# Kernel optimization log

Hardware: AMD Instinct MI355X
Metric: run time of the kernel (lower is better)

The kernel has to match this reference:

```python
import jax, jax.numpy as jnp
import numpy as np

LMAX = 6
NMAX = 5
RC = 6.0
N_ATOMS = 65536
L = LMAX + 1


def _solid_harmonics(p):
    """Orthonormal regular solid harmonics S_lm = r^l * Y_lm for one point p=(x,y,z),
    packed into an (L,L) matrix the way AutoForce's Ylm does:
      Y[l, l-m] = Re(S_lm)  (lower triangle incl. diagonal),
      Y[m-1, l] = Im(S_lm)  (strict upper triangle, m >= 1).
    These are polynomials in (x,y,z) so jacfwd gives exact analytic gradients."""
    x, y, z = p[0], p[1], p[2]
    r2 = x * x + y * y + z * z
    zero = jnp.zeros_like(x)
    re = {(0, 0): 0.28209479177387814 + zero}  # 1/sqrt(4*pi)
    im = {(0, 0): zero}
    for l in range(1, LMAX + 1):
        a = -float(np.sqrt((2 * l + 1) / (2.0 * l)))
        re[(l, l)] = a * (x * re[(l - 1, l - 1)] - y * im[(l - 1, l - 1)])
        im[(l, l)] = a * (x * im[(l - 1, l - 1)] + y * re[(l - 1, l - 1)])
        for m in range(l):
            A = float(np.sqrt((l * l - m * m) / ((2 * l - 1.0) * (2 * l + 1.0))))
            if l - 2 >= m:
                Ap = float(np.sqrt(((l - 1) ** 2 - m * m) / ((2 * l - 3.0) * (2 * l - 1.0))))
                re[(l, m)] = (z * re[(l - 1, m)] - Ap * r2 * re[(l - 2, m)]) / A
                im[(l, m)] = (z * im[(l - 1, m)] - Ap * r2 * im[(l - 2, m)]) / A
            else:
                re[(l, m)] = z * re[(l - 1, m)] / A
                im[(l, m)] = z * im[(l - 1, m)] / A
    rows = []
    for i in range(L):
        row = [re[(i, i - j)] if j <= i else im[(j, i + 1)] for j in range(L)]
        rows.append(jnp.stack(row))
    return jnp.stack(rows)  # (L, L)


def _radial(d):
    # PolyCut(RC): r(d) = (1 - d/rc)^2 for d < rc else 0, with analytic derivative.
    step = (d < RC).astype(d.dtype)
    t = 1.0 - d / RC
    return t * t * step, (-2.0 / RC) * t * step


def _masks(dtype):
    one = jnp.ones((L, L), dtype)
    Yr = 2.0 * jnp.tril(one) - jnp.eye(L, dtype=dtype)  # real-part mask
    Yi = 2.0 * jnp.triu(one, k=1)                        # imag-part mask
    return Yr, Yi


def setup_inputs() -> dict:
    key = jax.random.key(0)
    xyz = jax.random.normal(key, (N_ATOMS, 3), dtype=jnp.float32)
    return {"xyz": xyz}


def reference(xyz):
    Yr, Yi = _masks(xyz.dtype)
    d = jnp.sqrt(jnp.sum(xyz * xyz, axis=-1))                 # (N,)
    n = 2.0 * jnp.arange(NMAX + 1, dtype=xyz.dtype)           # (nm,) exponents 0,2,...,2*nmax
    r, dr = _radial(d)
    dpow = d[None, :] ** n[:, None]                           # (nm, N)
    f = r[None] * dpow                                        # (nm, N)

    Y = jax.vmap(_solid_harmonics)(xyz).transpose(1, 2, 0)                  # (L, L, N)
    dY = jax.vmap(jax.jacfwd(_solid_harmonics))(xyz).transpose(1, 2, 0, 3)  # (L, L, N, 3)

    c = jnp.einsum('nj,lmj->nlm', f, Y)                       # (nm, L, L)

    # p[a,b,l] = sum_m Yr[l,m] c[a,l,m] c[b,l,m];  Yi part indexed by column m.
    p = jnp.einsum('lm,alm,blm->abl', Yr, c, c) + jnp.einsum('lm,alm,blm->abm', Yi, c, c)

    # df/dd, then chain rule through d -> xyz; n=0 term vanishes (0 * d^-1, d>0).
    df = dr[None] * dpow + r[None] * n[:, None] * d[None] ** (n[:, None] - 1.0)  # (nm, N)
    dfv = df[:, :, None] * (xyz / d[:, None])[None]                              # (nm, N, 3)

    # dc[a,l,m,j,k] = dfv[a,j,k]*Y[l,m,j] + f[a,j]*dY[l,m,j,k]  (never materialized)
    # dp[a,b] = T[a,b] + T[b,a] with T = mask-contraction of dc[a]*c[b].
    G = jnp.einsum('lm,lmj,blm->blj', Yr, Y, c) + jnp.einsum('lm,lmj,blm->bmj', Yi, Y, c)        # (nm, L, N)
    H = jnp.einsum('lm,lmjk,blm->bljk', Yr, dY, c) + jnp.einsum('lm,lmjk,blm->bmjk', Yi, dY, c)  # (nm, L, N, 3)
    T = jnp.einsum('ajk,blj->abljk', dfv, G) + jnp.einsum('aj,bljk->abljk', f, H)                # (nm, nm, L, N, 3)
    dp = T + T.transpose(1, 0, 2, 3, 4)

    return p.transpose(2, 0, 1), dp.transpose(2, 0, 1, 3, 4)
```

## Files before the change

### kernel.cpp

```cpp
#include <hip/hip_runtime.h>
#include <math.h>

constexpr float C00f = 0.28209479177387814f;

constexpr float AL[7] = {0.f,
  -1.22474487139158905f, -1.11803398874989485f, -1.08012344973464354f,
  -1.06066017177982121f, -1.04880884817015154f, -1.04083299973306640f};

constexpr float AINV[7][7] = {
  {0,0,0,0,0,0,0},
  {1.73205080756887729f,0,0,0,0,0,0},
  {1.93649167310370852f,2.23606797749978969f,0,0,0,0,0},
  {1.97202659436653873f,2.09165006633518887f,2.64575131106459059f,0,0,0,0},
  {1.98431348329844304f,2.04939015319191986f,2.29128784747791999f,3.0f,0,0,0},
  {1.98997487421323993f,2.03100960115899020f,2.17124068443428311f,2.48746859276654987f,3.31662479035539985f,0,0},
  {1.99304345718356630f,2.02131499000000000f,2.11394180000000000f,2.30136840000000000f,2.67394840000000000f,3.60555127546398912f,0}
};

constexpr float APV[7][7] = {
  {0,0,0,0,0,0,0},
  {0,0,0,0,0,0,0},
  {0.57735026918962576f,0,0,0,0,0,0},
  {0.51639777949432225f,0.44721359549995794f,0,0,0,0,0},
  {0.50709255283710986f,0.47809144373375745f,0.37796447300922722f,0,0,0,0},
  {0.50395263067896967f,0.48795003647426655f,0.43643578047198484f,0.33333333333333333f,0,0,0},
  {0.50251890762960643f,0.49236596391733095f,0.46056618647183828f,0.40201512610368484f,0.30151134457776363f,0,0}
};

__global__ void k_zero(float* __restrict__ cg) {
  int t = blockIdx.x * 256 + threadIdx.x;
  if (t < 294) cg[t] = 0.f;
}

__device__ __forceinline__ void red32_acc(float v, float* dst, int li) {
  v += __shfl_xor(v,  1, 32);
  v += __shfl_xor(v,  2, 32);
  v += __shfl_xor(v,  4, 32);
  v += __shfl_xor(v,  8, 32);
  v += __shfl_xor(v, 16, 32);
  if (li == 0) atomicAdd(dst, v);
}

__global__ __launch_bounds__(256) void k_accum_c(const float* __restrict__ xyz,
                                                 float* __restrict__ cg, int n) {
  __shared__ float cl[294];
  for (int i = threadIdx.x; i < 294; i += 256) cl[i] = 0.f;
  __syncthreads();
  int lane = threadIdx.x & 63;
  int wv   = threadIdx.x >> 6;
  int li   = lane & 31;
  int half = lane >> 5;
  int atom = blockIdx.x * 128 + wv * 32 + li;
  int ji = (atom < n) ? atom : 0;
  float x = xyz[3*ji+0], y = xyz[3*ji+1], z = xyz[3*ji+2];
  float r2 = x*x + y*y + z*z;
  float d  = sqrtf(r2);
  float tcut = 1.f - d * (1.f/6.f);
  float r = (d < 6.f && atom < n) ? tcut*tcut : 0.f;
  float r2c  = r2*r2*r2;
  float base = half ? (r*r2c) : r;
  float fa[3];
  fa[0] = base; fa[1] = base*r2; fa[2] = fa[1]*r2;
  int abase = 3*half;

  float vr[2][7], vi[2][7];
  vr[0][0] = C00f; vi[0][0] = 0.f;
  #pragma unroll
  for (int l = 0; l <= 6; ++l) {
    const int cur = l & 1, prv = cur ^ 1;
    if (l > 0) {
      #pragma unroll
      for (int m = 0; m + 2 <= l; ++m) {
        float ai = AINV[l][m], ap = APV[l][m];
        vr[cur][m] = (z*vr[prv][m] - ap*r2*vr[cur][m]) * ai;
        vi[cur][m] = (z*vi[prv][m] - ap*r2*vi[cur][m]) * ai;
      }
      { float ai = AINV[l][l-1];
        float vpr = vr[prv][l-1], vpi = vi[prv][l-1];
        vr[cur][l-1] = z*vpr*ai;
        vi[cur][l-1] = z*vpi*ai;
        vr[cur][l] = AL[l]*(x*vpr - y*vpi);
        vi[cur][l] = AL[l]*(x*vpi + y*vpr); }
    }
    #pragma unroll
    for (int m = 0; m <= l; ++m) {
      int idx_re = l*7 + (l - m);
      #pragma unroll
      for (int i = 0; i < 3; ++i)
        red32_acc(fa[i]*vr[cur][m], &cl[(abase+i)*49 + idx_re], li);
      if (m >= 1) {
        int idx_im = (m-1)*7 + l;
        #pragma unroll
        for (int i = 0; i < 3; ++i)
          red32_acc(fa[i]*vi[cur][m], &cl[(abase+i)*49 + idx_im], li);
      }
    }
  }
  __syncthreads();
  for (int i = threadIdx.x; i < 294; i += 256) atomicAdd(&cg[i], cl[i]);
}

__global__ __launch_bounds__(256) void k_dp(const float* __restrict__ xyz,
                                            const float* __restrict__ cg,
                                            float* __restrict__ out, int n3) {
  __shared__ float cs[294];
  __shared__ __align__(16) float sbuf[36 * 256];
  for (int i = threadIdx.x; i < 294; i += 256) {
    int rc  = i % 49;
    int row = rc / 7, col = rc % 7;
    float wgt = (row == col) ? 1.f : 2.f;
    cs[i] = wgt * cg[i];
  }
  __syncthreads();

  if (blockIdx.x == 0 && threadIdx.x < 252) {
    int t = threadIdx.x;
    int pl = t / 36;
    int rem = t - 36*pl;
    int pa = rem / 6;
    int pb = rem - 6*pa;
    const float* ca = cg + pa*49;
    const float* cb = cg + pb*49;
    float s = 0.f;
    for (int mc = 0; mc <= pl; ++mc) {
      float wq = (mc == pl) ? 1.f : 2.f;
      s += wq * ca[pl*7+mc] * cb[pl*7+mc];
    }
    for (int rr = 0; rr < pl; ++rr)
      s += 2.f * ca[rr*7+pl] * cb[rr*7+pl];
    out[t] = s;
  }

  const int tx  = threadIdx.x;
  int tid = blockIdx.x * 256 + tx;
  int jj = (tid < n3) ? tid : (n3 - 1);
  int j = jj / 3;
  int k = jj - 3*j;
  float x = xyz[3*j+0], y = xyz[3*j+1], z = xyz[3*j+2];
  float ex = (k == 0) ? 1.f : 0.f;
  float ey = (k == 1) ? 1.f : 0.f;
  float ez = (k == 2) ? 1.f : 0.f;
  float pk = ex*x + ey*y + ez*z;
  float r2 = x*x + y*y + z*z;
  float d  = sqrtf(r2);
  float invd = (d > 0.f) ? 1.f/d : 0.f;
  bool inside = d < 6.f;
  float tcut = 1.f - d*(1.f/6.f);
  float r  = inside ? tcut*tcut : 0.f;
  float dr = inside ? (-1.f/3.f)*tcut : 0.f;
  float f[6], dfr[6];
  { float dp = 1.f;
    #pragma unroll
    for (int a = 0; a < 6; ++a) {
      f[a]   = r*dp;
      dfr[a] = dp*(dr + (2.f*a)*r*invd);
      dp *= r2;
    } }
  float w = pk * invd;
  float P[6];
  #pragma unroll
  for (int a = 0; a < 6; ++a) P[a] = dfr[a]*w;

  float* outdp = out + 252;
  const unsigned un3 = (unsigned)n3;
  const int sub = tx >> 6;
  const int ln  = tx & 63;
  const unsigned colbase = (unsigned)blockIdx.x * 256u + ((unsigned)ln << 2);
  const bool n3mul4 = (un3 & 3u) == 0u;

  float vr[2][7], vi[2][7], gr[2][7], gi[2][7];
  vr[0][0] = C00f; vi[0][0] = 0.f; gr[0][0] = 0.f; gi[0][0] = 0.f;
  #pragma unroll
  for (int l = 0; l <= 6; ++l) {
    const int cur = l & 1, prv = cur ^ 1;
    if (l > 0) {
      #pragma unroll
      for (int m = 0; m + 2 <= l; ++m) {
        float ai = AINV[l][m], ap = APV[l][m];
        float ovr = vr[cur][m], ovi = vi[cur][m];
        float ogr = gr[cur][m], ogi = gi[cur][m];
        vr[cur][m] = (z*vr[prv][m] - ap*r2*ovr) * ai;
        gr[cur][m] = (ez*vr[prv][m] + z*gr[prv][m] - ap*(2.f*pk*ovr + r2*ogr)) * ai;
        vi[cur][m] = (z*vi[prv][m] - ap*r2*ovi) * ai;
        gi[cur][m] = (ez*vi[prv][m] + z*gi[prv][m] - ap*(2.f*pk*ovi + r2*ogi)) * ai;
      }
      { float ai  = AINV[l][l-1];
        float vpr = vr[prv][l-1], vpi = vi[prv][l-1];
        float gpr = gr[prv][l-1], gpi = gi[prv][l-1];
        vr[cur][l-1] = z*vpr*ai;
        gr[cur][l-1] = (ez*vpr + z*gpr)*ai;
        vi[cur][l-1] = z*vpi*ai;
        gi[cur][l-1] = (ez*vpi + z*gpi)*ai;
        vr[cur][l] = AL[l]*(x*vpr - y*vpi);
        gr[cur][l] = AL[l]*(ex*vpr + x*gpr - ey*vpi - y*gpi);
        vi[cur][l] = AL[l]*(x*vpi + y*vpr);
        gi[cur][l] = AL[l]*(ex*vpi + x*gpi + ey*vpr + y*gpr); }
    }
    float G[6]  = {0,0,0,0,0,0};
    float Hh[6] = {0,0,0,0,0,0};
    #pragma unroll
    for (int m = 0; m <= l; ++m) {
      float vv = vr[cur][m], gg = gr[cur][m];
      int base = l*7 + (l - m);
      #pragma unroll
      for (int b = 0; b < 6; ++b) { float cc = cs[b*49 + base]; G[b] += vv*cc; Hh[b] += gg*cc; }
      if (m >= 1) {
        float vv2 = vi[cur][m], gg2 = gi[cur][m];
        int base2 = (m-1)*7 + l;
        #pragma unroll
        for (int b = 0; b < 6; ++b) { float cc = cs[b*49 + base2]; G[b] += vv2*cc; Hh[b] += gg2*cc; }
      }
    }
    #pragma unroll
    for (int a = 0; a < 6; ++a) {
      #pragma unroll
      for (int b = a; b < 6; ++b) {
        float val = P[a]*G[b] + f[a]*Hh[b] + P[b]*G[a] + f[b]*Hh[a];
        sbuf[(a*6 + b)*256 + tx] = val;
        if (b > a) sbuf[(b*6 + a)*256 + tx] = val;
      }
    }
    __syncthreads();
    #pragma unroll
    for (int g = 0; g < 9; ++g) {
      int p = g*4 + sub;
      const float* sp = &sbuf[p*256 + (ln << 2)];
      unsigned plane = (unsigned)(l*36 + p);
      if (n3mul4) {
        if (colbase + 4 <= un3) {
          float4 v = *reinterpret_cast<const float4*>(sp);
          *reinterpret_cast<float4*>(outdp + (size_t)plane * un3 + colbase) = v;
        }
      } else {
        #pragma unroll
        for (int q = 0; q < 4; ++q)
          if (colbase + q < un3)
            outdp[(size_t)plane * un3 + colbase + q] = sp[q];
      }
    }
    __syncthreads();
  }
}

extern "C" void kernel_launch(void* const* d_in, const int* in_sizes, int n_in,
                              void* d_out, int out_size, void* d_ws, size_t ws_size,
                              hipStream_t stream) {
  const float* xyz = (const float*)d_in[0];
  float* out = (float*)d_out;
  float* cg  = (float*)d_ws;
  int n3 = in_sizes[0];
  int n  = n3 / 3;

  k_zero   <<<dim3(2),               dim3(256), 0, stream>>>(cg);
  k_accum_c<<<dim3((n + 127)/128),   dim3(256), 0, stream>>>(xyz, cg, n);
  k_dp     <<<dim3((n3 + 255)/256),  dim3(256), 0, stream>>>(xyz, cg, out, n3);
}
```

Measured before the change: 245.3 us.

## Store symmetric dp tiles once and double-buffer shared staging in k_dp

Each shared staging buffer now keeps only the 21 unique symmetric (a,b) pairs rather than all 36, so half of the duplicate shared writes go away. The buffer is double-buffered by l parity, which drops the trailing barrier per l iteration. Blocks grow to 768 threads so each wave writes whole 3-row spans of a plane, and misaligned tails get a scalar fallback. The larger blocks and about 126KB of shared memory may limit occupancy to one block per CU.

```diff
diff --git a/kernel.cpp b/kernel.cpp
--- a/kernel.cpp
+++ b/kernel.cpp
@@ -26,6 +26,8 @@
   {0.50395263067896967f,0.48795003647426655f,0.43643578047198484f,0.33333333333333333f,0,0,0},
   {0.50251890762960643f,0.49236596391733095f,0.46056618647183828f,0.40201512610368484f,0.30151134457776363f,0,0}
 };
+
+#define IDX21(a,b) ((a)*(11-(a))/2 + (b))
 
 __global__ void k_zero(float* __restrict__ cg) {
   int t = blockIdx.x * 256 + threadIdx.x;
@@ -100,12 +102,13 @@
   for (int i = threadIdx.x; i < 294; i += 256) atomicAdd(&cg[i], cl[i]);
 }
 
-__global__ __launch_bounds__(256) void k_dp(const float* __restrict__ xyz,
+__global__ __launch_bounds__(768) void k_dp(const float* __restrict__ xyz,
                                             const float* __restrict__ cg,
                                             float* __restrict__ out, int n3) {
   __shared__ float cs[294];
-  __shared__ __align__(16) float sbuf[36 * 256];
-  for (int i = threadIdx.x; i < 294; i += 256) {
+  __shared__ __align__(16) float sbuf[2][21 * 768];
+  const int tx = threadIdx.x;
+  for (int i = tx; i < 294; i += 768) {
     int rc  = i % 49;
     int row = rc / 7, col = rc % 7;
     float wgt = (row == col) ? 1.f : 2.f;
@@ -113,8 +116,8 @@
   }
   __syncthreads();
 
-  if (blockIdx.x == 0 && threadIdx.x < 252) {
-    int t = threadIdx.x;
+  if (blockIdx.x == 0 && tx < 252) {
+    int t = tx;
     int pl = t / 36;
     int rem = t - 36*pl;
     int pa = rem / 6;
@@ -131,8 +134,7 @@
     out[t] = s;
   }
 
-  const int tx  = threadIdx.x;
-  int tid = blockIdx.x * 256 + tx;
+  int tid = blockIdx.x * 768 + tx;
   int jj = (tid < n3) ? tid : (n3 - 1);
   int j = jj / 3;
   int k = jj - 3*j;
@@ -148,25 +150,21 @@
   float tcut = 1.f - d*(1.f/6.f);
   float r  = inside ? tcut*tcut : 0.f;
   float dr = inside ? (-1.f/3.f)*tcut : 0.f;
-  float f[6], dfr[6];
+  float f[6], P[6];
+  float w = pk * invd;
   { float dp = 1.f;
     #pragma unroll
     for (int a = 0; a < 6; ++a) {
-      f[a]   = r*dp;
-      dfr[a] = dp*(dr + (2.f*a)*r*invd);
+      f[a] = r*dp;
+      P[a] = dp*(dr + (2.f*a)*r*invd) * w;
       dp *= r2;
     } }
-  float w = pk * invd;
-  float P[6];
-  #pragma unroll
-  for (int a = 0; a < 6; ++a) P[a] = dfr[a]*w;
 
   float* outdp = out + 252;
   const unsigned un3 = (unsigned)n3;
-  const int sub = tx >> 6;
+  const int wvi = tx >> 6;
   const int ln  = tx & 63;
-  const unsigned colbase = (unsigned)blockIdx.x * 256u + ((unsigned)ln << 2);
-  const bool n3mul4 = (un3 & 3u) == 0u;
+  const unsigned colblk = (unsigned)blockIdx.x * 768u;
 
   float vr[2][7], vi[2][7], gr[2][7], gi[2][7];
   vr[0][0] = C00f; vi[0][0] = 0.f; gr[0][0] = 0.f; gi[0][0] = 0.f;
@@ -211,34 +209,38 @@
         for (int b = 0; b < 6; ++b) { float cc = cs[b*49 + base2]; G[b] += vv2*cc; Hh[b] += gg2*cc; }
       }
     }
+    float* sb = sbuf[cur];
     #pragma unroll
     for (int a = 0; a < 6; ++a) {
       #pragma unroll
       for (int b = a; b < 6; ++b) {
         float val = P[a]*G[b] + f[a]*Hh[b] + P[b]*G[a] + f[b]*Hh[a];
-        sbuf[(a*6 + b)*256 + tx] = val;
-        if (b > a) sbuf[(b*6 + a)*256 + tx] = val;
+        sb[IDX21(a,b)*768 + tx] = val;
       }
     }
     __syncthreads();
     #pragma unroll
-    for (int g = 0; g < 9; ++g) {
-      int p = g*4 + sub;
-      const float* sp = &sbuf[p*256 + (ln << 2)];
-      unsigned plane = (unsigned)(l*36 + p);
-      if (n3mul4) {
-        if (colbase + 4 <= un3) {
-          float4 v = *reinterpret_cast<const float4*>(sp);
-          *reinterpret_cast<float4*>(outdp + (size_t)plane * un3 + colbase) = v;
+    for (int g = 0; g < 3; ++g) {
+      int p  = wvi*3 + g;
+      int pa = p / 6, pb = p - 6*pa;
+      int lo = pa < pb ? pa : pb;
+      int hi = pa < pb ? pb : pa;
+      const float* sp = &sb[IDX21(lo,hi)*768];
+      size_t planeoff = (size_t)(l*36 + p) * (size_t)un3;
+      #pragma unroll
+      for (int q = 0; q < 3; ++q) {
+        unsigned coff = (unsigned)(q*256 + (ln << 2));
+        unsigned col  = colblk + coff;
+        if (col + 4 <= un3) {
+          float4 v = *reinterpret_cast<const float4*>(sp + coff);
+          *reinterpret_cast<float4*>(outdp + planeoff + col) = v;
+        } else {
+          #pragma unroll
+          for (int qq = 0; qq < 4; ++qq)
+            if (col + qq < un3) outdp[planeoff + col + qq] = sp[coff + qq];
         }
-      } else {
-        #pragma unroll
-        for (int q = 0; q < 4; ++q)
-          if (colbase + q < un3)
-            outdp[(size_t)plane * un3 + colbase + q] = sp[q];
-      }
-    }
-    __syncthreads();
+      }
+    }
   }
 }
 
@@ -253,5 +255,5 @@
 
   k_zero   <<<dim3(2),               dim3(256), 0, stream>>>(cg);
   k_accum_c<<<dim3((n + 127)/128),   dim3(256), 0, stream>>>(xyz, cg, n);
-  k_dp     <<<dim3((n3 + 255)/256),  dim3(256), 0, stream>>>(xyz, cg, out, n3);
-}
+  k_dp     <<<dim3((n3 + 767)/768),  dim3(768), 0, stream>>>(xyz, cg, out, n3);
+}
```

Result: faster. 238.0 us (-3.0%).
